# Kernel tuning notes

Hardware: AMD Instinct MI355X
Metric: run time of the kernel (lower is better)

## Reference

```python
import jax, jax.numpy as jnp
import numpy as np

LN_EPS = 1e-5

def _layernorm(x, gamma, beta):
    # x: [B, 4, H]; gamma/beta: [4, H]; computed in fp32 as the torch subclass does
    x32 = x.astype(jnp.float32)
    mu = jnp.mean(x32, axis=-1, keepdims=True)
    var = jnp.mean(jnp.square(x32 - mu), axis=-1, keepdims=True)
    y = (x32 - mu) * jax.lax.rsqrt(var + LN_EPS)
    return (y * gamma + beta).astype(x.dtype)

def setup_inputs() -> dict:
    key = jax.random.key(0)
    ks = jax.random.split(key, 6)
    B, I, H = 8192, 512, 1024
    x = jax.random.normal(ks[0], (B, I), dtype=jnp.float32)
    h = jax.random.normal(ks[1], (B, H), dtype=jnp.float32)
    c = jax.random.normal(ks[2], (B, H), dtype=jnp.float32)
    Wi = jax.random.normal(ks[3], (I, 4 * H), dtype=jnp.float32) * (1.0 / np.sqrt(I))
    Wh = jax.random.normal(ks[4], (H, 4 * H), dtype=jnp.float32) * (1.0 / np.sqrt(H))
    bh = jax.random.normal(ks[5], (4 * H,), dtype=jnp.float32) * 0.01
    ln_gamma = jnp.ones((4, H), dtype=jnp.float32)
    ln_beta = jnp.zeros((4, H), dtype=jnp.float32)
    return {"x": x, "h": h, "c": c, "Wi": Wi, "Wh": Wh, "bh": bh,
            "ln_gamma": ln_gamma, "ln_beta": ln_beta}

def reference(x, h, c, Wi, Wh, bh, ln_gamma, ln_beta):
    B = x.shape[0]
    H = h.shape[-1]
    gates = x @ Wi + h @ Wh + bh            # [B, 4H]
    gates = gates.reshape(B, 4, H)           # chunk into i, f, g, o
    gates = _layernorm(gates, ln_gamma, ln_beta)
    i, f, g, o = gates[:, 0], gates[:, 1], gates[:, 2], gates[:, 3]
    c_new = jax.nn.sigmoid(f) * c + jax.nn.sigmoid(i) * jnp.tanh(g)
    h_new = jax.nn.sigmoid(o) * jnp.tanh(c_new)   # layer_norm_c is Identity
    return (h_new, c_new)
```

## Files before the change

### kernel.cpp

```cpp
#include <hip/hip_runtime.h>
#include <stdint.h>

#define BATCH 8192
#define IDIM  512
#define HDIM  1024
#define KDIM  1536
#define NDIM  4096
#define BK    64

typedef __bf16 bf16x8 __attribute__((ext_vector_type(8)));
typedef float  f32x4  __attribute__((ext_vector_type(4)));
typedef unsigned short u16x8 __attribute__((ext_vector_type(8)));

__device__ __forceinline__ unsigned short f2bf(float f) {
    union { float f; unsigned u; } v; v.f = f;
    unsigned r = v.u + 0x7fffu + ((v.u >> 16) & 1u);
    return (unsigned short)(r >> 16);
}
__device__ __forceinline__ float bf2f(unsigned short u) {
    union { unsigned u; float f; } v; v.u = ((unsigned)u) << 16;
    return v.f;
}
__device__ __forceinline__ float fexp(float x) {
    return __builtin_amdgcn_exp2f(x * 1.44269504f);
}
__device__ __forceinline__ float sigm(float x) {
    return __builtin_amdgcn_rcpf(1.f + fexp(-x));
}
__device__ __forceinline__ float ftanh(float x) {
    return 1.f - 2.f * __builtin_amdgcn_rcpf(1.f + fexp(2.f * x));
}

__device__ __forceinline__ void load16(void* lds, const void* g) {
    __builtin_amdgcn_global_load_lds(
        (const __attribute__((address_space(1))) unsigned int*)g,
        (__attribute__((address_space(3))) unsigned int*)lds, 16, 0, 0);
}

#define NPACKA (BATCH * KDIM / 4 / 256)
#define NPACKW ((NDIM / 32) * (KDIM / 32))
__global__ __launch_bounds__(256) void pack_ab(const float* __restrict__ x,
                                               const float* __restrict__ h,
                                               const float* __restrict__ Wi,
                                               const float* __restrict__ Wh,
                                               unsigned short* __restrict__ A,
                                               unsigned short* __restrict__ Wt) {
    __shared__ float tile[32][33];
    int blk = blockIdx.x;
    if (blk < NPACKA) {
        int idx = blk * 256 + threadIdx.x;
        int row = idx / (KDIM / 4);
        int g   = idx % (KDIM / 4);
        int col = g * 4;
        float4 v;
        if (col < IDIM) v = ((const float4*)(x + (size_t)row * IDIM))[g];
        else            v = ((const float4*)(h + (size_t)row * HDIM))[(col - IDIM) / 4];
        ushort4 o;
        o.x = f2bf(v.x); o.y = f2bf(v.y); o.z = f2bf(v.z); o.w = f2bf(v.w);
        ((ushort4*)A)[idx] = o;
    } else {
        int b  = blk - NPACKA;
        int n0 = (b & 127) * 32;
        int k0 = (b >> 7) * 32;
        int tx = threadIdx.x & 31, ty = threadIdx.x >> 5;
#pragma unroll
        for (int j = 0; j < 4; j++) {
            int k = k0 + ty + 8 * j;
            float v;
            if (k < IDIM) v = Wi[(size_t)k * NDIM + n0 + tx];
            else          v = Wh[(size_t)(k - IDIM) * NDIM + n0 + tx];
            tile[ty + 8 * j][tx] = v;
        }
        __syncthreads();
#pragma unroll
        for (int j = 0; j < 4; j++)
            Wt[(size_t)(n0 + ty + 8 * j) * KDIM + k0 + tx] = f2bf(tile[tx][ty + 8 * j]);
    }
}

__global__ __launch_bounds__(256) void gemm_bt(const unsigned short* __restrict__ A,
                                               const unsigned short* __restrict__ Bt,
                                               unsigned short* __restrict__ C) {
    __shared__ __align__(16) unsigned short sA[128 * BK];
    __shared__ __align__(16) unsigned short sB[128 * BK];

    const int t    = threadIdx.x;
    const int wave = t >> 6;
    const int lane = t & 63;
    const int bm   = blockIdx.x * 128;
    const int bn   = blockIdx.y * 128;

    const int wm   = (wave & 1) * 64;
    const int wn   = (wave >> 1) * 64;
    const int lrow = lane & 15;
    const int quad = lane >> 4;

    f32x4 acc[4][4] = {};

    int aofs[4], bofs[4];
#pragma unroll
    for (int s = 0; s < 4; s++) {
        int i = s * 256 + t;
        int r = i >> 3, pos = i & 7;
        int kc = pos ^ (r & 7);
        aofs[s] = (bm + r) * KDIM + kc * 8;
        bofs[s] = (bn + r) * KDIM + kc * 8;
    }

    int aoff[2][4], boff[2][4];
#pragma unroll
    for (int ss = 0; ss < 2; ss++)
#pragma unroll
        for (int i = 0; i < 4; i++) {
            int ra = wm + i * 16 + lrow;
            aoff[ss][i] = ra * BK + ((quad + 4 * ss) ^ (ra & 7)) * 8;
            int rb = wn + i * 16 + lrow;
            boff[ss][i] = rb * BK + ((quad + 4 * ss) ^ (rb & 7)) * 8;
        }

    for (int k0 = 0; k0 < KDIM; k0 += BK) {
#pragma unroll
        for (int s = 0; s < 4; s++) {
            load16(sA + s * 2048 + t * 8, A + (size_t)aofs[s] + k0);
            load16(sB + s * 2048 + t * 8, Bt + (size_t)bofs[s] + k0);
        }
        __syncthreads();

#pragma unroll
        for (int ss = 0; ss < 2; ss++) {
            bf16x8 af[4], bf[4];
#pragma unroll
            for (int mt = 0; mt < 4; mt++) af[mt] = *(const bf16x8*)(sA + aoff[ss][mt]);
#pragma unroll
            for (int nt = 0; nt < 4; nt++) bf[nt] = *(const bf16x8*)(sB + boff[ss][nt]);
#pragma unroll
            for (int mt = 0; mt < 4; mt++)
#pragma unroll
                for (int nt = 0; nt < 4; nt++)
                    acc[mt][nt] = __builtin_amdgcn_mfma_f32_16x16x32_bf16(
                        af[mt], bf[nt], acc[mt][nt], 0, 0, 0);
        }
        __syncthreads();
    }

#pragma unroll
    for (int mt = 0; mt < 4; mt++) {
#pragma unroll
        for (int nt = 0; nt < 4; nt++) {
            int row = bm + wm + mt * 16 + quad * 4;
            int col = bn + wn + nt * 16 + lrow;
#pragma unroll
            for (int r = 0; r < 4; r++)
                C[(size_t)(row + r) * NDIM + col] = f2bf(acc[mt][nt][r]);
        }
    }
}

__global__ __launch_bounds__(256) void lstm_ep(const unsigned short* __restrict__ gates,
                                               const float* __restrict__ bh,
                                               const float* __restrict__ c,
                                               const float* __restrict__ gamma,
                                               const float* __restrict__ beta,
                                               float* __restrict__ out) {
    const int wave = threadIdx.x >> 6;
    const int lane = threadIdx.x & 63;
    const int b    = blockIdx.x * 4 + wave;
    const int col0 = lane * 16;

    const unsigned short* gr = gates + (size_t)b * NDIM;
    float v[4][16];
    float s[4], sq[4];
#pragma unroll
    for (int g = 0; g < 4; g++) {
        const unsigned short* gp = gr + g * HDIM + col0;
        u16x8 ga = *(const u16x8*)gp;
        u16x8 gb = *(const u16x8*)(gp + 8);
        float bb[16];
#pragma unroll
        for (int q = 0; q < 4; q++)
            *(float4*)(bb + 4 * q) = ((const float4*)(bh + g * HDIM + col0))[q];
        float ls = 0.f, lq = 0.f;
#pragma unroll
        for (int j = 0; j < 16; j++) {
            float tv = bf2f(j < 8 ? ga[j] : gb[j - 8]) + bb[j];
            v[g][j] = tv; ls += tv; lq += tv * tv;
        }
        s[g] = ls; sq[g] = lq;
    }
#pragma unroll
    for (int off = 32; off; off >>= 1) {
#pragma unroll
        for (int g = 0; g < 4; g++) {
            s[g]  += __shfl_xor(s[g], off);
            sq[g] += __shfl_xor(sq[g], off);
        }
    }
#pragma unroll
    for (int g = 0; g < 4; g++) {
        const float mu  = s[g] * (1.f / HDIM);
        const float var = sq[g] * (1.f / HDIM) - mu * mu;
        const float rs  = rsqrtf(var + 1e-5f);
        float gm[16], bt[16];
#pragma unroll
        for (int q = 0; q < 4; q++) {
            *(float4*)(gm + 4 * q) = ((const float4*)(gamma + g * HDIM + col0))[q];
            *(float4*)(bt + 4 * q) = ((const float4*)(beta  + g * HDIM + col0))[q];
        }
#pragma unroll
        for (int j = 0; j < 16; j++) {
            float y = (v[g][j] - mu) * rs * gm[j] + bt[j];
            v[g][j] = (g == 2) ? ftanh(y) : sigm(y);
        }
    }
    const size_t base = (size_t)b * HDIM + col0;
#pragma unroll
    for (int q = 0; q < 4; q++) {
        float4 ci = *(const float4*)(c + base + 4 * q);
        float4 cn, hn;
#pragma unroll
        for (int e = 0; e < 4; e++) {
            int j = 4 * q + e;
            float cnv = v[1][j] * ((float*)&ci)[e] + v[0][j] * v[2][j];
            ((float*)&cn)[e] = cnv;
            ((float*)&hn)[e] = v[3][j] * ftanh(cnv);
        }
        *(float4*)(out + base + 4 * q) = hn;
        *(float4*)(out + (size_t)BATCH * HDIM + base + 4 * q) = cn;
    }
}

extern "C" void kernel_launch(void* const* d_in, const int* in_sizes, int n_in,
                              void* d_out, int out_size, void* d_ws, size_t ws_size,
                              hipStream_t stream) {
    const float* x     = (const float*)d_in[0];
    const float* h     = (const float*)d_in[1];
    const float* c     = (const float*)d_in[2];
    const float* Wi    = (const float*)d_in[3];
    const float* Wh    = (const float*)d_in[4];
    const float* bh    = (const float*)d_in[5];
    const float* gamma = (const float*)d_in[6];
    const float* beta  = (const float*)d_in[7];
    float* out = (float*)d_out;

    unsigned short* A  = (unsigned short*)d_ws;
    unsigned short* Wt = (unsigned short*)((char*)d_ws + (size_t)BATCH * KDIM * 2);
    unsigned short* gates = (unsigned short*)((char*)d_ws + (size_t)BATCH * KDIM * 2
                                                          + (size_t)NDIM * KDIM * 2);

    pack_ab<<<NPACKA + NPACKW, 256, 0, stream>>>(x, h, Wi, Wh, A, Wt);
    gemm_bt<<<dim3(BATCH / 128, NDIM / 128), 256, 0, stream>>>(A, Wt, gates);
    lstm_ep<<<BATCH / 4, 256, 0, stream>>>(gates, bh, c, gamma, beta, out);
}
```

Before: 310.0 us.

## Rewrite GEMM with 256x256 tiles, 4-stage async LDS pipeline and block swizzle

Replaces the 128x128 single-buffered GEMM with a 256x256 tile computed by 512 threads. It uses a 4-deep ring of 32-wide K stages in 128KB LDS with explicit vmcnt waits and barriers, so global loads overlap MFMA work. Each wave computes 128x64, MFMA bursts run at raised priority, and blocks are swizzled for L2 reuse. The LDS footprint is large and allows one block per CU despite launch_bounds(512,2). The hand-counted vmcnt values must match how the compiler lowers load16.

```diff
diff --git a/kernel.cpp b/kernel.cpp
--- a/kernel.cpp
+++ b/kernel.cpp
@@ -6,7 +6,6 @@
 #define HDIM  1024
 #define KDIM  1536
 #define NDIM  4096
-#define BK    64
 
 typedef __bf16 bf16x8 __attribute__((ext_vector_type(8)));
 typedef float  f32x4  __attribute__((ext_vector_type(4)));
@@ -78,73 +77,109 @@
     }
 }
 
-__global__ __launch_bounds__(256) void gemm_bt(const unsigned short* __restrict__ A,
-                                               const unsigned short* __restrict__ Bt,
-                                               unsigned short* __restrict__ C) {
-    __shared__ __align__(16) unsigned short sA[128 * BK];
-    __shared__ __align__(16) unsigned short sB[128 * BK];
+__global__ __launch_bounds__(512, 2) void gemm_bt(const unsigned short* __restrict__ A,
+                                                  const unsigned short* __restrict__ Bt,
+                                                  unsigned short* __restrict__ C) {
+    __shared__ __align__(16) unsigned short smem[65536];
 
     const int t    = threadIdx.x;
     const int wave = t >> 6;
     const int lane = t & 63;
-    const int bm   = blockIdx.x * 128;
-    const int bn   = blockIdx.y * 128;
-
-    const int wm   = (wave & 1) * 64;
-    const int wn   = (wave >> 1) * 64;
     const int lrow = lane & 15;
     const int quad = lane >> 4;
 
-    f32x4 acc[4][4] = {};
-
-    int aofs[4], bofs[4];
-#pragma unroll
-    for (int s = 0; s < 4; s++) {
-        int i = s * 256 + t;
-        int r = i >> 3, pos = i & 7;
-        int kc = pos ^ (r & 7);
-        aofs[s] = (bm + r) * KDIM + kc * 8;
-        bofs[s] = (bn + r) * KDIM + kc * 8;
-    }
-
-    int aoff[2][4], boff[2][4];
-#pragma unroll
-    for (int ss = 0; ss < 2; ss++)
-#pragma unroll
-        for (int i = 0; i < 4; i++) {
-            int ra = wm + i * 16 + lrow;
-            aoff[ss][i] = ra * BK + ((quad + 4 * ss) ^ (ra & 7)) * 8;
-            int rb = wn + i * 16 + lrow;
-            boff[ss][i] = rb * BK + ((quad + 4 * ss) ^ (rb & 7)) * 8;
-        }
-
-    for (int k0 = 0; k0 < KDIM; k0 += BK) {
-#pragma unroll
-        for (int s = 0; s < 4; s++) {
-            load16(sA + s * 2048 + t * 8, A + (size_t)aofs[s] + k0);
-            load16(sB + s * 2048 + t * 8, Bt + (size_t)bofs[s] + k0);
-        }
-        __syncthreads();
-
-#pragma unroll
-        for (int ss = 0; ss < 2; ss++) {
-            bf16x8 af[4], bf[4];
-#pragma unroll
-            for (int mt = 0; mt < 4; mt++) af[mt] = *(const bf16x8*)(sA + aoff[ss][mt]);
-#pragma unroll
-            for (int nt = 0; nt < 4; nt++) bf[nt] = *(const bf16x8*)(sB + boff[ss][nt]);
-#pragma unroll
-            for (int mt = 0; mt < 4; mt++)
-#pragma unroll
-                for (int nt = 0; nt < 4; nt++)
-                    acc[mt][nt] = __builtin_amdgcn_mfma_f32_16x16x32_bf16(
-                        af[mt], bf[nt], acc[mt][nt], 0, 0, 0);
-        }
-        __syncthreads();
-    }
-
-#pragma unroll
-    for (int mt = 0; mt < 4; mt++) {
+    const int bid = blockIdx.x;
+    const int swz = (bid & 7) * 64 + (bid >> 3);
+    const int bm  = (swz & 31) * 256;
+    const int bn  = (swz >> 5) * 256;
+
+    const int wm = (wave & 1) * 128;
+    const int wn = (wave >> 1) * 64;
+
+    int srcA[2], srcB[2];
+#pragma unroll
+    for (int j = 0; j < 2; j++) {
+        int q   = t + 512 * j;
+        int rp  = q >> 3, s = q & 7;
+        int xx  = s ^ (rp & 7);
+        int row = 2 * rp + (xx >> 2);
+        int kc  = xx & 3;
+        srcA[j] = (bm + row) * KDIM + kc * 8;
+        srcB[j] = (bn + row) * KDIM + kc * 8;
+    }
+
+    int offA[8], offB[4];
+#pragma unroll
+    for (int mt = 0; mt < 8; mt++) {
+        int r = wm + mt * 16 + lrow;
+        offA[mt] = (r >> 1) * 64 + (((((r & 1) << 2) | quad) ^ ((r >> 1) & 7)) * 8);
+    }
+#pragma unroll
+    for (int nt = 0; nt < 4; nt++) {
+        int r = wn + nt * 16 + lrow;
+        offB[nt] = (r >> 1) * 64 + (((((r & 1) << 2) | quad) ^ ((r >> 1) & 7)) * 8);
+    }
+
+    f32x4 acc[8][4] = {};
+
+#define STAGE(tt) do {                                              \
+    unsigned short* _d = smem + (((tt) & 3) << 14);                 \
+    const int _ko = (tt) * 32;                                      \
+    load16(_d +          t * 8, A  + (size_t)(srcA[0] + _ko));      \
+    load16(_d +  4096 +  t * 8, A  + (size_t)(srcA[1] + _ko));      \
+    load16(_d +  8192 +  t * 8, Bt + (size_t)(srcB[0] + _ko));      \
+    load16(_d + 12288 +  t * 8, Bt + (size_t)(srcB[1] + _ko));      \
+} while (0)
+
+    STAGE(0); STAGE(1); STAGE(2);
+
+    const int NT = KDIM / 32;
+    for (int T = 0; T < NT; ++T) {
+        if (T < NT - 2)       asm volatile("s_waitcnt vmcnt(8)" ::: "memory");
+        else if (T == NT - 2) asm volatile("s_waitcnt vmcnt(4)" ::: "memory");
+        else                  asm volatile("s_waitcnt vmcnt(0)" ::: "memory");
+        __builtin_amdgcn_s_barrier();
+        asm volatile("" ::: "memory");
+
+        const unsigned short* bufA = smem + ((T & 3) << 14);
+        const unsigned short* bufB = bufA + 8192;
+
+        bf16x8 a[4], b[4];
+#pragma unroll
+        for (int i = 0; i < 4; i++) a[i] = *(const bf16x8*)(bufA + offA[i]);
+#pragma unroll
+        for (int i = 0; i < 4; i++) b[i] = *(const bf16x8*)(bufB + offB[i]);
+        if (T + 3 < NT) STAGE(T + 3);
+
+        __builtin_amdgcn_s_barrier();
+        __builtin_amdgcn_s_setprio(1);
+#pragma unroll
+        for (int mt = 0; mt < 4; mt++)
+#pragma unroll
+            for (int nt = 0; nt < 4; nt++)
+                acc[mt][nt] = __builtin_amdgcn_mfma_f32_16x16x32_bf16(
+                    a[mt], b[nt], acc[mt][nt], 0, 0, 0);
+        __builtin_amdgcn_s_setprio(0);
+        __builtin_amdgcn_s_barrier();
+
+        bf16x8 a2[4];
+#pragma unroll
+        for (int i = 0; i < 4; i++) a2[i] = *(const bf16x8*)(bufA + offA[4 + i]);
+
+        __builtin_amdgcn_s_barrier();
+        __builtin_amdgcn_s_setprio(1);
+#pragma unroll
+        for (int mt = 0; mt < 4; mt++)
+#pragma unroll
+            for (int nt = 0; nt < 4; nt++)
+                acc[4 + mt][nt] = __builtin_amdgcn_mfma_f32_16x16x32_bf16(
+                    a2[mt], b[nt], acc[4 + mt][nt], 0, 0, 0);
+        __builtin_amdgcn_s_setprio(0);
+    }
+#undef STAGE
+
+#pragma unroll
+    for (int mt = 0; mt < 8; mt++)
 #pragma unroll
         for (int nt = 0; nt < 4; nt++) {
             int row = bm + wm + mt * 16 + quad * 4;
@@ -153,7 +188,6 @@
             for (int r = 0; r < 4; r++)
                 C[(size_t)(row + r) * NDIM + col] = f2bf(acc[mt][nt][r]);
         }
-    }
 }
 
 __global__ __launch_bounds__(256) void lstm_ep(const unsigned short* __restrict__ gates,
@@ -248,6 +282,6 @@
                                                           + (size_t)NDIM * KDIM * 2);
 
     pack_ab<<<NPACKA + NPACKW, 256, 0, stream>>>(x, h, Wi, Wh, A, Wt);
-    gemm_bt<<<dim3(BATCH / 128, NDIM / 128), 256, 0, stream>>>(A, Wt, gates);
+    gemm_bt<<<dim3((BATCH / 256) * (NDIM / 256)), 512, 0, stream>>>(A, Wt, gates);
     lstm_ep<<<BATCH / 4, 256, 0, stream>>>(gates, bh, c, gamma, beta, out);
 }
```

Measured after the change: 308.1 us. No clear change (-0.6%).
